# Performance work log

Measured on AMD Instinct MI355X. Metric: run time of the kernel, lower is better.

The kernel has to match this reference:

```python
import jax, jax.numpy as jnp
import numpy as np

DIM = 1024
N_HEADS = 16
HEAD_DIM = DIM // N_HEADS
HIDDEN = 4096  # round_up(4*DIM, 256)
ROPE_THETA = 10000.0
EPS = 1e-6


def setup_inputs() -> dict:
    key = jax.random.key(0)
    ks = jax.random.split(key, 10)
    s = 0.02
    return {
        "x": jax.random.normal(ks[0], (1, 4096, DIM), dtype=jnp.float32),
        "wq": jax.random.normal(ks[1], (DIM, DIM), dtype=jnp.float32) * s,
        "wk": jax.random.normal(ks[2], (DIM, DIM), dtype=jnp.float32) * s,
        "wv": jax.random.normal(ks[3], (DIM, DIM), dtype=jnp.float32) * s,
        "wo": jax.random.normal(ks[4], (DIM, DIM), dtype=jnp.float32) * s,
        "w1": jax.random.normal(ks[5], (HIDDEN, DIM), dtype=jnp.float32) * s,
        "w2": jax.random.normal(ks[6], (DIM, HIDDEN), dtype=jnp.float32) * s,
        "w3": jax.random.normal(ks[7], (HIDDEN, DIM), dtype=jnp.float32) * s,
        "g_attn": jnp.ones((DIM,), dtype=jnp.float32),
        "g_ffn": jnp.ones((DIM,), dtype=jnp.float32),
    }


def _rmsnorm(x, g):
    return x * jax.lax.rsqrt(jnp.mean(x * x, axis=-1, keepdims=True) + EPS) * g


def _rope_tables(seqlen):
    inv = 1.0 / (ROPE_THETA ** (jnp.arange(0, HEAD_DIM, 2, dtype=jnp.float32) / HEAD_DIM))
    ang = jnp.arange(seqlen, dtype=jnp.float32)[:, None] * inv[None, :]  # [s, hd/2]
    return jnp.cos(ang), jnp.sin(ang)


def _apply_rope(q, cos, sin):
    # q: [b, s, h, hd]; pairs (even, odd) treated as complex (re, im)
    b, s, h, d = q.shape
    qr = q.reshape(b, s, h, d // 2, 2)
    re, im = qr[..., 0], qr[..., 1]
    c = cos[None, :, None, :]
    sn = sin[None, :, None, :]
    out = jnp.stack([re * c - im * sn, re * sn + im * c], axis=-1)
    return out.reshape(b, s, h, d)


def reference(x, wq, wk, wv, wo, w1, w2, w3, g_attn, g_ffn):
    b, s, _ = x.shape
    xn = _rmsnorm(x, g_attn)
    q = (xn @ wq.T).reshape(b, s, N_HEADS, HEAD_DIM)
    k = (xn @ wk.T).reshape(b, s, N_HEADS, HEAD_DIM)
    v = (xn @ wv.T).reshape(b, s, N_HEADS, HEAD_DIM)
    cos, sin = _rope_tables(s)
    q = _apply_rope(q, cos, sin)
    k = _apply_rope(k, cos, sin)
    scores = jnp.einsum("bthd,bThd->bhtT", q, k) / np.sqrt(HEAD_DIM).astype(np.float32)
    probs = jax.nn.softmax(scores, axis=-1)
    attn = jnp.einsum("bhtT,bThd->bthd", probs, v).reshape(b, s, DIM)
    h = x + attn @ wo.T
    hn = _rmsnorm(h, g_ffn)
    ff = (jax.nn.silu(hn @ w1.T) * (hn @ w3.T)) @ w2.T
    return h + ff
```

## Files before the change

kernel.cpp:

```cpp
#include <hip/hip_runtime.h>

#define S_LEN 4096
#define DIMM  1024
#define NH    16
#define HD    64
#define HID   4096

typedef unsigned short u16;
typedef __attribute__((ext_vector_type(8))) short bf16x8;
typedef __attribute__((ext_vector_type(4))) short short4b;
typedef __attribute__((ext_vector_type(8))) unsigned short u16x8;
typedef __attribute__((ext_vector_type(4))) float f32x4;

__device__ __forceinline__ u16 f2bf(float f) {
  unsigned u = __float_as_uint(f);
  u += 0x7fffu + ((u >> 16) & 1u);
  return (u16)(u >> 16);
}
__device__ __forceinline__ float bf2f(u16 h) {
  return __uint_as_float(((unsigned)h) << 16);
}
__device__ __forceinline__ unsigned pack_bf16(float hi, float lo) {
  return __builtin_amdgcn_perm(__float_as_uint(hi), __float_as_uint(lo), 0x07060302u);
}
__device__ __forceinline__ float fexp2(float x) { return __builtin_amdgcn_exp2f(x); }

__device__ __forceinline__ void gl_lds16(const void* g, void* l) {
  __builtin_amdgcn_global_load_lds(
      (const __attribute__((address_space(1))) void*)g,
      (__attribute__((address_space(3))) void*)l, 16, 0, 0);
}

__global__ __launch_bounds__(256) void prep_kernel(
    const float* __restrict__ wq, const float* __restrict__ wk, const float* __restrict__ wv,
    const float* __restrict__ wo, const float* __restrict__ w1, const float* __restrict__ w3,
    const float* __restrict__ w2, const float* __restrict__ x, const float* __restrict__ g_attn,
    u16* __restrict__ wqkb, u16* __restrict__ wvb, u16* __restrict__ wob,
    u16* __restrict__ w13b, u16* __restrict__ w2b, u16* __restrict__ xnb,
    float* __restrict__ cosT, float* __restrict__ sinT) {
  int b = blockIdx.x;
  int t = threadIdx.x;
  if (b < 8192) {
    const float* src;
    u16* dst;
    int i;
    if (b < 2048) {
      int which = b >> 9, lb = b & 511;
      src = which == 0 ? wq : which == 1 ? wk : which == 2 ? wv : wo;
      dst = which == 0 ? wqkb : which == 1 ? (wqkb + (1 << 20)) : which == 2 ? wvb : wob;
      i = (lb * 256 + t) * 8;
    } else {
      int b2 = b - 2048, which = b2 >> 11, lb = b2 & 2047;
      src = which == 0 ? w1 : which == 1 ? w3 : w2;
      dst = which == 0 ? w13b : which == 1 ? (w13b + (4 << 20)) : w2b;
      i = (lb * 256 + t) * 8;
    }
    float4 a = *(const float4*)(src + i);
    float4 c = *(const float4*)(src + i + 4);
    u16x8 r;
    r[0] = f2bf(a.x); r[1] = f2bf(a.y); r[2] = f2bf(a.z); r[3] = f2bf(a.w);
    r[4] = f2bf(c.x); r[5] = f2bf(c.y); r[6] = f2bf(c.z); r[7] = f2bf(c.w);
    *(u16x8*)(dst + i) = r;
  } else if (b < 8704) {
    int idx = (b - 8192) * 256 + t;
    int pos = idx >> 5, i = idx & 31;
    double inv = pow(10000.0, -(double)(2 * i) / 64.0);
    double a = (double)pos * inv;
    cosT[idx] = (float)cos(a);
    sinT[idx] = (float)sin(a);
  } else {
    int row = b - 8704;
    const float4 v = *(const float4*)(x + (size_t)row * DIMM + t * 4);
    float ss = v.x * v.x + v.y * v.y + v.z * v.z + v.w * v.w;
#pragma unroll
    for (int off = 32; off > 0; off >>= 1) ss += __shfl_down(ss, off);
    __shared__ float red[4];
    if ((t & 63) == 0) red[t >> 6] = ss;
    __syncthreads();
    float tot = red[0] + red[1] + red[2] + red[3];
    float sc = rsqrtf(tot * (1.0f / DIMM) + 1e-6f);
    const float4 gv = *(const float4*)(g_attn + t * 4);
    ushort4 o;
    o.x = f2bf(v.x * sc * gv.x);
    o.y = f2bf(v.y * sc * gv.y);
    o.z = f2bf(v.z * sc * gv.z);
    o.w = f2bf(v.w * sc * gv.w);
    *(ushort4*)(xnb + (size_t)row * DIMM + t * 4) = o;
  }
}

__global__ __launch_bounds__(256) void rmsnorm_kernel(const float* __restrict__ x, const float* __restrict__ g,
                                                      u16* __restrict__ out) {
  int row = blockIdx.x;
  int t = threadIdx.x;
  const float4 v = *(const float4*)(x + (size_t)row * DIMM + t * 4);
  float ss = v.x * v.x + v.y * v.y + v.z * v.z + v.w * v.w;
#pragma unroll
  for (int off = 32; off > 0; off >>= 1) ss += __shfl_down(ss, off);
  __shared__ float red[4];
  if ((t & 63) == 0) red[t >> 6] = ss;
  __syncthreads();
  float tot = red[0] + red[1] + red[2] + red[3];
  float sc = rsqrtf(tot * (1.0f / DIMM) + 1e-6f);
  const float4 gv = *(const float4*)(g + t * 4);
  ushort4 o;
  o.x = f2bf(v.x * sc * gv.x);
  o.y = f2bf(v.y * sc * gv.y);
  o.z = f2bf(v.z * sc * gv.z);
  o.w = f2bf(v.w * sc * gv.w);
  *(ushort4*)(out + (size_t)row * DIMM + t * 4) = o;
}

template <int OUTMODE>
__global__ __launch_bounds__(512) void gemm_kernel(const u16* __restrict__ A, const u16* __restrict__ B,
                                                   void* Cout, const float* res, int N, int K, int lda,
                                                   int ldb, const float* cosT, const float* sinT) {
  __shared__ uint4 As0[1024], Bs0[1024], As1[1024], Bs1[1024];
  const int t = threadIdx.x;
  const int w = t >> 6, l = t & 63;
  const int wm = w >> 1, wn = w & 1;
  const int bm = blockIdx.y, bn = blockIdx.x;
  const int quad = l >> 4, lc = l & 15;

  f32x4 acc[2][4];
  const f32x4 zero = {0.0f, 0.0f, 0.0f, 0.0f};
#pragma unroll
  for (int mi = 0; mi < 2; mi++)
#pragma unroll
    for (int ni = 0; ni < 4; ni++) acc[mi][ni] = zero;

  const int band0 = t >> 6, kq0 = (t >> 4) & 3, row0 = t & 15;
  const u16* Ap0 = A + (size_t)(bm * 128 + band0 * 16 + row0) * lda + kq0 * 8;
  const u16* Bp0 = B + (size_t)(bn * 128 + band0 * 16 + row0) * ldb + kq0 * 8;
  if constexpr (OUTMODE == 4) {
    Ap0 += (size_t)blockIdx.z * K;
    Bp0 += (size_t)blockIdx.z * K;
  }
  const int abase = wm * 128 + l;
  const int bbase = wn * 256 + l;

#define STAGEL(AD, BD, K0)                 \
  do {                                     \
    gl_lds16(Ap0 + (K0), &(AD)[t]);        \
    gl_lds16(Ap0 + (K0) + 32, &(AD)[t + 512]); \
    gl_lds16(Bp0 + (K0), &(BD)[t]);        \
    gl_lds16(Bp0 + (K0) + 32, &(BD)[t + 512]); \
  } while (0)

#define COMPL(AS, BS)                                                                               \
  do {                                                                                              \
    _Pragma("unroll") for (int ks = 0; ks < 2; ks++) {                                              \
      bf16x8 af[2], bfr[4];                                                                         \
      _Pragma("unroll") for (int mi = 0; mi < 2; mi++)                                              \
          af[mi] = *(const bf16x8*)&(AS)[ks * 512 + abase + mi * 64];                               \
      _Pragma("unroll") for (int ni = 0; ni < 4; ni++)                                              \
          bfr[ni] = *(const bf16x8*)&(BS)[ks * 512 + bbase + ni * 64];                              \
      _Pragma("unroll") for (int mi = 0; mi < 2; mi++)                                              \
          _Pragma("unroll") for (int ni = 0; ni < 4; ni++)                                          \
              acc[mi][ni] = __builtin_amdgcn_mfma_f32_16x16x32_bf16(af[mi], bfr[ni], acc[mi][ni], 0, 0, 0); \
    }                                                                                               \
  } while (0)

  STAGEL(As0, Bs0, 0);
  __syncthreads();
  int k0 = 0;
  for (; k0 + 128 < K; k0 += 128) {
    STAGEL(As1, Bs1, k0 + 64);
    COMPL(As0, Bs0);
    __syncthreads();
    STAGEL(As0, Bs0, k0 + 128);
    COMPL(As1, Bs1);
    __syncthreads();
  }
  STAGEL(As1, Bs1, k0 + 64);
  COMPL(As0, Bs0);
  __syncthreads();
  COMPL(As1, Bs1);
#undef STAGEL
#undef COMPL

  const int rbase = bm * 128 + wm * 32 + quad * 4;
  const int cbase = bn * 128 + wn * 64 + lc;
  const float qs = (OUTMODE == 3 && bn < 8) ? 0.18033688011112f : 1.0f;
#pragma unroll
  for (int mi = 0; mi < 2; mi++) {
#pragma unroll
    for (int r = 0; r < 4; r++) {
      int row = rbase + mi * 16 + r;
#pragma unroll
      for (int ni = 0; ni < 4; ni++) {
        int col = cbase + ni * 16;
        if constexpr (OUTMODE == 0) {
          ((u16*)Cout)[(size_t)row * N + col] = f2bf(acc[mi][ni][r]);
        } else if constexpr (OUTMODE == 1) {
          size_t idx = (size_t)row * N + col;
          ((float*)Cout)[idx] = res[idx] + acc[mi][ni][r];
        } else if constexpr (OUTMODE == 2) {
          int h = row >> 6, din = row & 63;
          int kb = col >> 6, k63 = col & 63;
          int off = ((h << 6) + kb) * 4096 + (((din >> 4) << 1) + (k63 >> 5)) * 512 +
                    ((((k63 >> 2) & 3) << 4) + (din & 15)) * 8 + ((k63 >> 4) & 1) * 4 + (k63 & 3);
          ((u16*)Cout)[off] = f2bf(acc[mi][ni][r]);
        } else if constexpr (OUTMODE == 4) {
          size_t idx = (size_t)row * N + col;
          atomicAdd((float*)Cout + idx, acc[mi][ni][r]);
        } else {
          float v = acc[mi][ni][r];
          float pv = __shfl_xor(v, 1);
          int i = ((ni * 16 + lc) & 63) >> 1;
          float c = cosT[(row << 5) + i], s = sinT[(row << 5) + i];
          float o = (lc & 1) ? (pv * s + v * c) : (v * c - pv * s);
          ((u16*)Cout)[(size_t)row * N + col] = f2bf(o * qs);
        }
      }
    }
  }
}

__global__ __launch_bounds__(512) void gemm256_kernel(const u16* __restrict__ A, const u16* __restrict__ B,
                                                      u16* __restrict__ Cout, int N, int K, int lda) {
  __shared__ uint4 As0[1024], Bs0[1024], As1[1024], Bs1[1024], As2[1024], Bs2[1024];
  const int t = threadIdx.x;
  const int w = t >> 6, l = t & 63;
  const int wm = w >> 2, wn = w & 3;
  const int bm = blockIdx.y, bn = blockIdx.x;
  const int quad = l >> 4, lc = l & 15;

  f32x4 acc[8][4];
  const f32x4 zero = {0.0f, 0.0f, 0.0f, 0.0f};
#pragma unroll
  for (int mi = 0; mi < 8; mi++)
#pragma unroll
    for (int ni = 0; ni < 4; ni++) acc[mi][ni] = zero;

  const int band0 = t >> 6, kq0 = (t >> 4) & 3, row0 = t & 15;
  const u16* Ap0 = A + (size_t)(bm * 256 + band0 * 16 + row0) * lda + kq0 * 8;
  const u16* Bp0 = B + (size_t)(bn * 256 + band0 * 16 + row0) * K + kq0 * 8;
  const size_t Astep = (size_t)128 * lda;
  const size_t Bstep = (size_t)128 * K;

#define STG(AD, BD, K0)                           \
  do {                                            \
    gl_lds16(Ap0 + (K0), &(AD)[t]);               \
    gl_lds16(Ap0 + Astep + (K0), &(AD)[t + 512]); \
    gl_lds16(Bp0 + (K0), &(BD)[t]);               \
    gl_lds16(Bp0 + Bstep + (K0), &(BD)[t + 512]); \
  } while (0)

  const int NT = K >> 5;

#define PHASE(CA, CB, SA, SB, TT)                                              \
  do {                                                                         \
    if ((TT) + 2 < NT) STG(SA, SB, ((TT) + 2) * 32);                           \
    bf16x8 af[8], bfr[4];                                                      \
    _Pragma("unroll") for (int mi = 0; mi < 8; mi++)                           \
        af[mi] = *(const bf16x8*)&(CA)[(wm * 8 + mi) * 64 + l];                \
    _Pragma("unroll") for (int ni = 0; ni < 4; ni++)                           \
        bfr[ni] = *(const bf16x8*)&(CB)[(wn * 4 + ni) * 64 + l];               \
    __builtin_amdgcn_s_setprio(1);                                             \
    _Pragma("unroll") for (int mi = 0; mi < 8; mi++)                           \
        _Pragma("unroll") for (int ni = 0; ni < 4; ni++)                       \
            acc[mi][ni] = __builtin_amdgcn_mfma_f32_16x16x32_bf16(af[mi], bfr[ni], acc[mi][ni], 0, 0, 0); \
    __builtin_amdgcn_s_setprio(0);                                             \
    if ((TT) + 1 < NT) {                                                       \
      asm volatile("s_waitcnt lgkmcnt(0)" ::: "memory");                       \
      if ((TT) + 2 < NT) {                                                     \
        asm volatile("s_waitcnt vmcnt(4)" ::: "memory");                       \
      } else {                                                                 \
        asm volatile("s_waitcnt vmcnt(0)" ::: "memory");                       \
      }                                                                        \
      __builtin_amdgcn_s_barrier();                                            \
    }                                                                          \
  } while (0)

  STG(As0, Bs0, 0);
  STG(As1, Bs1, 32);
  asm volatile("s_waitcnt vmcnt(4)" ::: "memory");
  __builtin_amdgcn_s_barrier();

  for (int tt = 0; tt < NT; tt += 3) {
    PHASE(As0, Bs0, As2, Bs2, tt);
    if (tt + 1 < NT) PHASE(As1, Bs1, As0, Bs0, tt + 1);
    if (tt + 2 < NT) PHASE(As2, Bs2, As1, Bs1, tt + 2);
  }
#undef STG
#undef PHASE

  const int rbase = bm * 256 + wm * 128 + quad * 4;
  const int cbase = bn * 256 + wn * 64 + lc;
#pragma unroll
  for (int mi = 0; mi < 8; mi++) {
#pragma unroll
    for (int r = 0; r < 4; r++) {
      int row = rbase + mi * 16 + r;
#pragma unroll
      for (int ni = 0; ni < 4; ni++) {
        int col = cbase + ni * 16;
        Cout[(size_t)row * N + col] = f2bf(acc[mi][ni][r]);
      }
    }
  }
}

__global__ __launch_bounds__(512) void attn_kernel(const u16* __restrict__ Qm, const u16* __restrict__ Km,
                                                   const u16* __restrict__ Vsw, u16* __restrict__ Om) {
  __shared__ char smem[32768];
  uint4* Ks0 = (uint4*)smem;
  uint4* Vs0 = (uint4*)(smem + 8192);
  uint4* Ks1 = (uint4*)(smem + 16384);
  uint4* Vs1 = (uint4*)(smem + 24576);
  const int t = threadIdx.x;
  const int w = t >> 6, l = t & 63;
  const int quad = l >> 4, lc = l & 15;
  const int hd = blockIdx.y;
  const int qrow = blockIdx.x * 128 + w * 16;

  bf16x8 qf_[2];
#pragma unroll
  for (int ch = 0; ch < 2; ch++)
    qf_[ch] = *(const bf16x8*)(Qm + (size_t)(qrow + lc) * 2048 + hd * HD + ch * 32 + quad * 8);

  const f32x4 zero = {0.0f, 0.0f, 0.0f, 0.0f};
  const bf16x8 ones8 = {(short)0x3F80, (short)0x3F80, (short)0x3F80, (short)0x3F80,
                        (short)0x3F80, (short)0x3F80, (short)0x3F80, (short)0x3F80};
  f32x4 Oa[4];
#pragma unroll
  for (int df = 0; df < 4; df++) Oa[df] = zero;
  f32x4 lsacc = zero;

  const int s0 = t >> 7, c0 = (t >> 6) & 1, kq0 = (t >> 4) & 3, row0 = t & 15;
  const u16* Kp0 = Km + (size_t)(s0 * 16 + row0) * 2048 + hd * HD + c0 * 32 + kq0 * 8;
  const u16* Vp = Vsw + (size_t)(hd * HD) * 4096 + t * 8;

#define STAGEKV(KD, VD, TT)                                  \
  do {                                                       \
    gl_lds16(Kp0 + (size_t)(TT)*131072, &(KD)[t]);           \
    gl_lds16(Vp + (size_t)(TT)*4096, &(VD)[t]);              \
  } while (0)

#define TILE_COMPUTE(KS, VS)                                                                 \
  do {                                                                                       \
    f32x4 Sf[4];                                                                             \
    _Pragma("unroll") for (int kf = 0; kf < 4; kf++) {                                       \
      bf16x8 ka = *(const bf16x8*)&(KS)[kf * 128 + l];                                       \
      bf16x8 kb2 = *(const bf16x8*)&(KS)[kf * 128 + 64 + l];                                 \
      f32x4 z = __builtin_amdgcn_mfma_f32_16x16x32_bf16(ka, qf_[0], zero, 0, 0, 0);          \
      z = __builtin_amdgcn_mfma_f32_16x16x32_bf16(kb2, qf_[1], z, 0, 0, 0);                  \
      Sf[kf] = z;                                                                            \
    }                                                                                        \
    _Pragma("unroll") for (int kf = 0; kf < 4; kf++)                                         \
        _Pragma("unroll") for (int r = 0; r < 4; r++)                                        \
      Sf[kf][r] = fexp2(Sf[kf][r]);                                                          \
    union { bf16x8 v8; uint2 u2[2]; } p0, p1;                                                \
    p0.u2[0].x = pack_bf16(Sf[0][1], Sf[0][0]);                                              \
    p0.u2[0].y = pack_bf16(Sf[0][3], Sf[0][2]);                                              \
    p0.u2[1].x = pack_bf16(Sf[1][1], Sf[1][0]);                                              \
    p0.u2[1].y = pack_bf16(Sf[1][3], Sf[1][2]);                                              \
    p1.u2[0].x = pack_bf16(Sf[2][1], Sf[2][0]);                                              \
    p1.u2[0].y = pack_bf16(Sf[2][3], Sf[2][2]);                                              \
    p1.u2[1].x = pack_bf16(Sf[3][1], Sf[3][0]);                                              \
    p1.u2[1].y = pack_bf16(Sf[3][3], Sf[3][2]);                                              \
    lsacc = __builtin_amdgcn_mfma_f32_16x16x32_bf16(ones8, p0.v8, lsacc, 0, 0, 0);           \
    lsacc = __builtin_amdgcn_mfma_f32_16x16x32_bf16(ones8, p1.v8, lsacc, 0, 0, 0);           \
    _Pragma("unroll") for (int df = 0; df < 4; df++) {                                       \
      bf16x8 va = *(const bf16x8*)&(VS)[(df * 2) * 64 + l];                                  \
      bf16x8 vb = *(const bf16x8*)&(VS)[(df * 2 + 1) * 64 + l];                              \
      Oa[df] = __builtin_amdgcn_mfma_f32_16x16x32_bf16(va, p0.v8, Oa[df], 0, 0, 0);          \
      Oa[df] = __builtin_amdgcn_mfma_f32_16x16x32_bf16(vb, p1.v8, Oa[df], 0, 0, 0);          \
    }                                                                                        \
  } while (0)

  STAGEKV(Ks0, Vs0, 0);
  __syncthreads();

  for (int tt = 0; tt < 64; tt += 2) {
    STAGEKV(Ks1, Vs1, tt + 1);
    TILE_COMPUTE(Ks0, Vs0);
    __syncthreads();
    if (tt + 2 < 64) STAGEKV(Ks0, Vs0, tt + 2);
    TILE_COMPUTE(Ks1, Vs1);
    __syncthreads();
  }
#undef STAGEKV
#undef TILE_COMPUTE

  u16* ep = (u16*)smem;
  float invl = 1.0f / lsacc[0];
#pragma unroll
  for (int df = 0; df < 4; df++) {
    int qb = w * 16 + lc;
    int d = df * 16 + quad * 4;
    uint2 pv;
    pv.x = pack_bf16(Oa[df][1] * invl, Oa[df][0] * invl);
    pv.y = pack_bf16(Oa[df][3] * invl, Oa[df][2] * invl);
    *(uint2*)(ep + qb * 72 + d) = pv;
  }
  __syncthreads();
#pragma unroll
  for (int it = 0; it < 2; it++) {
    int qb = it * 64 + (t >> 3);
    int dp = (t & 7) * 8;
    u16x8 rowv = *(const u16x8*)(ep + qb * 72 + dp);
    *(u16x8*)(Om + (size_t)(blockIdx.x * 128 + qb) * DIMM + hd * HD + dp) = rowv;
  }
}

__global__ __launch_bounds__(256) void silu_mul_kernel(u16* __restrict__ u13) {
  int i = (blockIdx.x * 256 + threadIdx.x) * 8;
  int r = i >> 12, c = i & 4095;
  u16* up = u13 + (size_t)r * 8192 + c;
  u16x8 uv = *(const u16x8*)up;
  u16x8 gv = *(const u16x8*)(up + 4096);
  u16x8 o;
#pragma unroll
  for (int j = 0; j < 8; j++) {
    float a = bf2f(uv[j]);
    float b = bf2f(gv[j]);
    float sv = a / (1.0f + __expf(-a));
    o[j] = f2bf(sv * b);
  }
  *(u16x8*)up = o;
}

extern "C" void kernel_launch(void* const* d_in, const int* in_sizes, int n_in,
                              void* d_out, int out_size, void* d_ws, size_t ws_size,
                              hipStream_t stream) {
  const float* x      = (const float*)d_in[0];
  const float* wq     = (const float*)d_in[1];
  const float* wk     = (const float*)d_in[2];
  const float* wv     = (const float*)d_in[3];
  const float* wo     = (const float*)d_in[4];
  const float* w1     = (const float*)d_in[5];
  const float* w2     = (const float*)d_in[6];
  const float* w3     = (const float*)d_in[7];
  const float* g_attn = (const float*)d_in[8];
  const float* g_ffn  = (const float*)d_in[9];
  float* out = (float*)d_out;
  char* ws = (char*)d_ws;
  const size_t MB = 1ull << 20;

  u16* wqkb = (u16*)(ws + 0 * MB);
  u16* wvb  = (u16*)(ws + 4 * MB);
  u16* wob  = (u16*)(ws + 6 * MB);
  u16* w13b = (u16*)(ws + 8 * MB);
  u16* w2b  = (u16*)(ws + 24 * MB);
  u16* xnb  = (u16*)(ws + 32 * MB);
  u16* qkb  = (u16*)(ws + 40 * MB);
  u16* vswz = (u16*)(ws + 56 * MB);
  u16* attb = (u16*)(ws + 64 * MB);
  u16* u13  = (u16*)(ws + 40 * MB);
  float* cosT = (float*)(ws + 104 * MB);
  float* sinT = (float*)(ws + 104 * MB + 512 * 1024);

  prep_kernel<<<12800, 256, 0, stream>>>(wq, wk, wv, wo, w1, w3, w2, x, g_attn,
                                         wqkb, wvb, wob, w13b, w2b, xnb, cosT, sinT);

  gemm_kernel<3><<<dim3(16, 32), 512, 0, stream>>>(xnb, wqkb, qkb, nullptr, 2048, DIMM, DIMM, DIMM, cosT, sinT);
  gemm_kernel<2><<<dim3(32, 8), 512, 0, stream>>>(wvb, xnb, vswz, nullptr, S_LEN, DIMM, DIMM, DIMM, nullptr, nullptr);

  attn_kernel<<<dim3(32, 16), 512, 0, stream>>>(qkb, qkb + 1024, vswz, attb);

  gemm_kernel<1><<<dim3(8, 32), 512, 0, stream>>>(attb, wob, out, x, DIMM, DIMM, DIMM, DIMM, nullptr, nullptr);

  rmsnorm_kernel<<<4096, 256, 0, stream>>>(out, g_ffn, xnb);

  gemm256_kernel<<<dim3(32, 16), 512, 0, stream>>>(xnb, w13b, u13, 8192, DIMM, DIMM);

  silu_mul_kernel<<<8192, 256, 0, stream>>>(u13);

  gemm_kernel<4><<<dim3(8, 32, 2), 512, 0, stream>>>(u13, w2b, out, nullptr, DIMM, 2048, 8192, HID, nullptr, nullptr);
}
```

Measured before the change: 483.1 us.

## Deepen GEMM LDS pipeline to four stages and double-buffer fragment registers

The 256x256 GEMM kernel moves from a three-buffer to a four-buffer LDS ring, so global-to-LDS loads are issued three tiles ahead instead of two. It also double-buffers the MFMA operand fragments in registers: the next tile's LDS reads are issued before the current tile's MFMAs, so LDS latency overlaps with matrix math. The cost is more LDS per block (128KB) and roughly double the fragment registers, which adds register pressure and could cause spills or lower occupancy.

Result: slower. 494.4 us (+2.3%).

```diff
diff --git a/kernel.cpp b/kernel.cpp
--- a/kernel.cpp
+++ b/kernel.cpp
@@ -219,7 +219,8 @@
 
 __global__ __launch_bounds__(512) void gemm256_kernel(const u16* __restrict__ A, const u16* __restrict__ B,
                                                       u16* __restrict__ Cout, int N, int K, int lda) {
-  __shared__ uint4 As0[1024], Bs0[1024], As1[1024], Bs1[1024], As2[1024], Bs2[1024];
+  __shared__ uint4 As0[1024], Bs0[1024], As1[1024], Bs1[1024],
+                   As2[1024], Bs2[1024], As3[1024], Bs3[1024];
   const int t = threadIdx.x;
   const int w = t >> 6, l = t & 63;
   const int wm = w >> 2, wn = w & 3;
@@ -247,24 +248,35 @@
     gl_lds16(Bp0 + Bstep + (K0), &(BD)[t + 512]); \
   } while (0)
 
+#define RDREG(AF, BF, AS, BS)                                                  \
+  do {                                                                         \
+    _Pragma("unroll") for (int mi = 0; mi < 8; mi++)                           \
+        AF[mi] = *(const bf16x8*)&(AS)[(wm * 8 + mi) * 64 + l];                \
+    _Pragma("unroll") for (int ni = 0; ni < 4; ni++)                           \
+        BF[ni] = *(const bf16x8*)&(BS)[(wn * 4 + ni) * 64 + l];                \
+  } while (0)
+
+#define MMA(AF, BF)                                                                                 \
+  do {                                                                                              \
+    __builtin_amdgcn_s_setprio(1);                                                                  \
+    _Pragma("unroll") for (int mi = 0; mi < 8; mi++)                                                \
+        _Pragma("unroll") for (int ni = 0; ni < 4; ni++)                                            \
+            acc[mi][ni] = __builtin_amdgcn_mfma_f32_16x16x32_bf16(AF[mi], BF[ni], acc[mi][ni], 0, 0, 0); \
+    __builtin_amdgcn_s_setprio(0);                                                                  \
+  } while (0)
+
   const int NT = K >> 5;
 
-#define PHASE(CA, CB, SA, SB, TT)                                              \
+  bf16x8 afA[8], bfA[4], afB[8], bfB[4];
+
+#define PH(TT, CURA, CURB, NXTA, NXTB, SA, SB, RA_, RB_)                       \
   do {                                                                         \
-    if ((TT) + 2 < NT) STG(SA, SB, ((TT) + 2) * 32);                           \
-    bf16x8 af[8], bfr[4];                                                      \
-    _Pragma("unroll") for (int mi = 0; mi < 8; mi++)                           \
-        af[mi] = *(const bf16x8*)&(CA)[(wm * 8 + mi) * 64 + l];                \
-    _Pragma("unroll") for (int ni = 0; ni < 4; ni++)                           \
-        bfr[ni] = *(const bf16x8*)&(CB)[(wn * 4 + ni) * 64 + l];               \
-    __builtin_amdgcn_s_setprio(1);                                             \
-    _Pragma("unroll") for (int mi = 0; mi < 8; mi++)                           \
-        _Pragma("unroll") for (int ni = 0; ni < 4; ni++)                       \
-            acc[mi][ni] = __builtin_amdgcn_mfma_f32_16x16x32_bf16(af[mi], bfr[ni], acc[mi][ni], 0, 0, 0); \
-    __builtin_amdgcn_s_setprio(0);                                             \
+    if ((TT) + 3 < NT) STG(SA, SB, ((TT) + 3) * 32);                           \
+    if ((TT) + 1 < NT) RDREG(NXTA, NXTB, RA_, RB_);                            \
+    MMA(CURA, CURB);                                                           \
     if ((TT) + 1 < NT) {                                                       \
       asm volatile("s_waitcnt lgkmcnt(0)" ::: "memory");                       \
-      if ((TT) + 2 < NT) {                                                     \
+      if ((TT) + 3 < NT) {                                                     \
         asm volatile("s_waitcnt vmcnt(4)" ::: "memory");                       \
       } else {                                                                 \
         asm volatile("s_waitcnt vmcnt(0)" ::: "memory");                       \
@@ -275,16 +287,23 @@
 
   STG(As0, Bs0, 0);
   STG(As1, Bs1, 32);
+  STG(As2, Bs2, 64);
   asm volatile("s_waitcnt vmcnt(4)" ::: "memory");
   __builtin_amdgcn_s_barrier();
-
-  for (int tt = 0; tt < NT; tt += 3) {
-    PHASE(As0, Bs0, As2, Bs2, tt);
-    if (tt + 1 < NT) PHASE(As1, Bs1, As0, Bs0, tt + 1);
-    if (tt + 2 < NT) PHASE(As2, Bs2, As1, Bs1, tt + 2);
+  RDREG(afA, bfA, As0, Bs0);
+  asm volatile("s_waitcnt lgkmcnt(0)" ::: "memory");
+  __builtin_amdgcn_s_barrier();
+
+  for (int tt = 0; tt < NT; tt += 4) {
+    PH(tt,     afA, bfA, afB, bfB, As3, Bs3, As1, Bs1);
+    PH(tt + 1, afB, bfB, afA, bfA, As0, Bs0, As2, Bs2);
+    PH(tt + 2, afA, bfA, afB, bfB, As1, Bs1, As3, Bs3);
+    PH(tt + 3, afB, bfB, afA, bfA, As2, Bs2, As0, Bs0);
   }
 #undef STG
-#undef PHASE
+#undef RDREG
+#undef MMA
+#undef PH
 
   const int rbase = bm * 256 + wm * 128 + quad * 4;
   const int cbase = bn * 256 + wn * 64 + lc;
```
